# Kernel optimization log

Measured on AMD Instinct MI355X. Metric: run time of the kernel, lower is better.

## Reference

```python
import jax, jax.numpy as jnp
import numpy as np

TEMP = 0.07
LOSS_WEIGHT = 0.01
QSIZE = 1024


def _l2norm(x, axis):
    # torch: x / clamp_min(norm(x, dim=axis, keepdim=True), 1e-5)
    return x / jnp.maximum(jnp.linalg.norm(x, axis=axis, keepdims=True), 1e-5)


def setup_inputs() -> dict:
    key = jax.random.key(0)
    k1, k2, k3, k4 = jax.random.split(key, 4)
    B, E, H, W, C = 2, 256, 32, 32, 80
    feature = jax.random.normal(k1, (B, E, H, W), jnp.float32)
    u = jax.random.uniform(k2, (B, C, H, W), jnp.float32)
    center_map = jnp.where(u > 0.99, u, 0.0)
    score_map = jax.random.normal(k3, (B, C, H, W), jnp.float32)
    # buffer init: normalize(randn(Q,E,C), dim=1) / 10
    q = jax.random.normal(k4, (QSIZE, E, C), jnp.float32)
    queue = q / jnp.clip(jnp.linalg.norm(q, axis=1, keepdims=True), 1e-12) / 10.0
    return {"feature": feature, "center_map": center_map, "score_map": score_map, "queue": queue}


def reference(feature, center_map, score_map, queue):
    B, E, H, W = feature.shape
    C = score_map.shape[1]
    Class = center_map.shape[1]  # == C (required by the original assert)
    HW = H * W
    Q = queue.shape[0]  # steady state: queue_is_full -> Q = queue_size

    # score_map already at (H, W); nearest interpolate is identity
    sm = jax.lax.stop_gradient(score_map.reshape(B, C, HW).transpose(0, 2, 1))  # (B,HW,C)
    sm = jax.nn.softmax(sm / 0.001, axis=-1)
    cm = jax.lax.stop_gradient(center_map.reshape(B, Class, HW).transpose(0, 2, 1))  # (B,HW,Class)

    feat = feature.reshape(B, E, HW)
    # per-class prototypes from softmaxed score map, L2-normalized over E
    cate_protos = _l2norm(jnp.einsum('beh,bhc->bec', feat, sm), axis=1)  # (B,E,C)
    # update_queue: swap oldest batch (ptr=0) with detached current prototypes
    queue = queue.at[:B].set(jax.lax.stop_gradient(cate_protos))  # (Q,E,C)

    pos_proto = _l2norm(jnp.einsum('beh,bhk->bek', feat, cm), axis=1)  # (B,E,Class)
    feat_n = _l2norm(feat, axis=1)  # (B,E,HW)

    # feat_neg_score: (B, HW, Q, C); column (q,c) of the original (E, Q*C) view
    neg = jnp.einsum('beh,qec->bhqc', feat_n, queue) / TEMP
    pos = jnp.einsum('beh,bek->bhk', feat_n, pos_proto) / TEMP  # (B,HW,Class)

    # logsumexp over queue slots per class column
    s = jax.scipy.special.logsumexp(neg, axis=2)  # (B,HW,C)
    # for class cls, negatives exclude all columns with c == cls (pos_idx mask)
    eye = jnp.eye(C, dtype=bool)  # (cls, c)
    s_excl = jnp.where(eye[None, None], -jnp.inf, s[:, :, None, :])  # (B,HW,cls,c)
    lse_neg = jax.scipy.special.logsumexp(s_excl, axis=-1)  # (B,HW,C)
    # concat logits = [l_pos, masked negs]; total logsumexp
    lse_total = jnp.logaddexp(pos, lse_neg)  # (B,HW,C)

    # labels = cls (faithful to original code): in the concat ordering, index cls is
    # l_pos for cls==0, else masked-neg column (q=0, c=cls-1)
    tgt = jnp.concatenate([pos[:, :, :1], neg[:, :, 0, :C - 1]], axis=-1)  # (B,HW,C)
    ce = lse_total - tgt  # per-pixel, per-class CE

    mask = (cm > 0).astype(ce.dtype)  # (B,HW,Class)
    cnt = mask.sum(axis=(0, 1))  # (Class,)
    per_cls = jnp.where(cnt > 0, (ce * mask).sum(axis=(0, 1)) / jnp.maximum(cnt, 1.0), 0.0)
    return LOSS_WEIGHT * per_cls.sum()
```

## Files before the change

kernel.cpp:

```cpp
#include <hip/hip_runtime.h>
#include <hip/hip_bf16.h>


#define B_ 2
#define E_ 256
#define HW_ 1024
#define C_ 80
#define Q_ 1024

typedef __attribute__((ext_vector_type(4))) float f32x4;
typedef __attribute__((ext_vector_type(8))) short bf16x8;
typedef unsigned int u32;
typedef __attribute__((ext_vector_type(4))) u32 u32x4;

#define L2E 1.4426950408889634f
#define SCALE_A (L2E / 0.07f)
#define INV_TEMP (1.0f / 0.07f)

__device__ __forceinline__ ushort f2bf(float f) {
  union { __hip_bfloat16 b; ushort u; } cv;
  cv.b = __float2bfloat16(f);
  return cv.u;
}

__device__ __forceinline__ void gload_lds16(const short* g, short* l) {
  __builtin_amdgcn_global_load_lds(
      (const __attribute__((address_space(1))) void*)g,
      (__attribute__((address_space(3))) void*)l, 16, 0, 0);
}

__device__ __forceinline__ float wred_sum(float v) {
#pragma unroll
  for (int m = 1; m < 64; m <<= 1) v += __shfl_xor(v, m, 64);
  return v;
}

__global__ void k_sm(const float* __restrict__ score, float* __restrict__ SM,
                     float* __restrict__ CSUM, float* __restrict__ CCNT) {
  __shared__ float ld[80][33];
  __shared__ float red[8][32];
  __shared__ float mstore[32], istore[32];
  int t = threadIdx.x;
  if (blockIdx.x == 0 && t < C_) { CSUM[t] = 0.f; CCNT[t] = 0.f; }
  int p0 = blockIdx.x * 32;
  int b = p0 >> 10, h0 = p0 & 1023;
#pragma unroll
  for (int j = 0; j < 3; j++) {
    int idx = j*256 + t;
    if (idx < 640) {
      int row = idx >> 3, c4 = idx & 7;
      float4 v = *(const float4*)(score + ((size_t)(b*C_ + row))*HW_ + h0 + c4*4);
      ld[row][c4*4+0] = v.x; ld[row][c4*4+1] = v.y;
      ld[row][c4*4+2] = v.z; ld[row][c4*4+3] = v.w;
    }
  }
  __syncthreads();
  int px = t & 31, wg = t >> 5;
  float m = -__builtin_inff();
  for (int c = wg*10; c < wg*10 + 10; c++) m = fmaxf(m, ld[c][px]);
  red[wg][px] = m;
  __syncthreads();
  if (t < 32) {
    float mm = red[0][t];
#pragma unroll
    for (int g = 1; g < 8; g++) mm = fmaxf(mm, red[g][t]);
    mstore[t] = mm;
  }
  __syncthreads();
  float mf = mstore[px];
  float s = 0.f;
  for (int c = wg*10; c < wg*10 + 10; c++)
    s += __builtin_amdgcn_exp2f((ld[c][px] - mf) * (1000.0f * L2E));
  red[wg][px] = s;
  __syncthreads();
  if (t < 32) {
    float ss = 0.f;
#pragma unroll
    for (int g = 0; g < 8; g++) ss += red[g][t];
    istore[t] = 1.0f / ss;
  }
  __syncthreads();
#pragma unroll
  for (int j = 0; j < 3; j++) {
    int idx = j*256 + t;
    if (idx < 640) {
      int wpx = idx / 20, c4 = idx % 20;
      float mf2 = mstore[wpx], iv = istore[wpx];
      float4 o;
      o.x = __builtin_amdgcn_exp2f((ld[c4*4+0][wpx] - mf2) * (1000.0f * L2E)) * iv;
      o.y = __builtin_amdgcn_exp2f((ld[c4*4+1][wpx] - mf2) * (1000.0f * L2E)) * iv;
      o.z = __builtin_amdgcn_exp2f((ld[c4*4+2][wpx] - mf2) * (1000.0f * L2E)) * iv;
      o.w = __builtin_amdgcn_exp2f((ld[c4*4+3][wpx] - mf2) * (1000.0f * L2E)) * iv;
      *(float4*)(SM + (size_t)(p0 + wpx)*C_ + c4*4) = o;
    }
  }
}

__global__ void k_featn(const float* __restrict__ feat, float* __restrict__ FEATN,
                        float* __restrict__ NORM, __hip_bfloat16* __restrict__ ABF) {
  __shared__ float ld[256][33];
  __shared__ float red[8][32];
  __shared__ float istore[32];
  int t = threadIdx.x;
  int p0 = blockIdx.x * 32;
  int b = p0 >> 10, h0 = p0 & 1023;
#pragma unroll
  for (int j = 0; j < 8; j++) {
    int idx = j*256 + t;
    int row = idx >> 3, c4 = idx & 7;
    float4 v = *(const float4*)(feat + ((size_t)(b*E_ + row))*HW_ + h0 + c4*4);
    ld[row][c4*4+0] = v.x; ld[row][c4*4+1] = v.y;
    ld[row][c4*4+2] = v.z; ld[row][c4*4+3] = v.w;
  }
  __syncthreads();
  int px = t & 31, wg = t >> 5;
  float s = 0.f;
  for (int e = wg*32; e < wg*32 + 32; e++) { float v = ld[e][px]; s += v*v; }
  red[wg][px] = s;
  __syncthreads();
  if (t < 32) {
    float ss = 0.f;
#pragma unroll
    for (int g = 0; g < 8; g++) ss += red[g][t];
    float nrm = sqrtf(ss);
    NORM[p0 + t] = nrm;
    istore[t] = 1.0f / fmaxf(nrm, 1e-5f);
  }
  __syncthreads();
#pragma unroll
  for (int j = 0; j < 8; j++) {
    int idx = j*256 + t;
    int wpx = idx >> 6, e4 = idx & 63;
    float iv = istore[wpx];
    float f0 = ld[e4*4+0][wpx] * iv;
    float f1 = ld[e4*4+1][wpx] * iv;
    float f2 = ld[e4*4+2][wpx] * iv;
    float f3 = ld[e4*4+3][wpx] * iv;
    float4 o; o.x = f0; o.y = f1; o.z = f2; o.w = f3;
    *(float4*)(FEATN + (size_t)(p0 + wpx)*E_ + e4*4) = o;
    ushort4 pk;
    pk.x = f2bf(f0 * SCALE_A); pk.y = f2bf(f1 * SCALE_A);
    pk.z = f2bf(f2 * SCALE_A); pk.w = f2bf(f3 * SCALE_A);
    *(ushort4*)((ushort*)ABF + (size_t)(p0 + wpx)*E_ + e4*4) = pk;
  }
}

__global__ void k_protos(const float* __restrict__ SM, const float* __restrict__ cmap,
                         const float* __restrict__ FEATN, const float* __restrict__ NORM,
                         float* __restrict__ PART) {
  int hch = blockIdx.x, b = blockIdx.y;
  int map = blockIdx.z >> 1, ch = blockIdx.z & 1;
  int e = threadIdx.x;
  __shared__ float wl[64][40];
  for (int idx = threadIdx.x; idx < 64*40; idx += 256) {
    int ii = idx / 40, cl = idx % 40;
    int c = ch*40 + cl;
    int p = b*HW_ + hch*64 + ii;
    int h = p & 1023;
    float wv = (map == 0) ? SM[(size_t)p*C_ + c] : cmap[((size_t)(b*C_ + c))*HW_ + h];
    wl[ii][cl] = wv * NORM[p];
  }
  __syncthreads();
  float acc[40];
#pragma unroll
  for (int j = 0; j < 40; j++) acc[j] = 0.f;
  for (int ii = 0; ii < 64; ii++) {
    int p = b*HW_ + hch*64 + ii;
    float f = FEATN[(size_t)p*E_ + e];
#pragma unroll
    for (int j = 0; j < 40; j++) acc[j] += f * wl[ii][j];
  }
  float* out = PART + ((size_t)(hch*4 + map*2 + b)*E_ + e)*C_ + ch*40;
#pragma unroll
  for (int j = 0; j < 40; j++) out[j] = acc[j];
}

__global__ void k_protred(const float* __restrict__ PART, float* __restrict__ PROT) {
  int g = blockIdx.x*256 + threadIdx.x;
  float s = 0.f;
#pragma unroll 8
  for (int chk = 0; chk < 32; chk++) s += PART[(size_t)chk*81920 + g];
  PROT[g] = s;
}

__global__ void k_norm(float* PROT) {
  int w = threadIdx.x >> 6, l = threadIdx.x & 63;
  int gid = blockIdx.x*4 + w;
  int mb = gid / C_, c = gid % C_;
  float v[4]; float ss = 0.f;
#pragma unroll
  for (int i = 0; i < 4; i++) {
    v[i] = PROT[((size_t)(mb*E_ + l + 64*i))*C_ + c];
    ss += v[i]*v[i];
  }
  ss = wred_sum(ss);
  float inv = 1.0f / fmaxf(sqrtf(ss), 1e-5f);
#pragma unroll
  for (int i = 0; i < 4; i++)
    PROT[((size_t)(mb*E_ + l + 64*i))*C_ + c] = v[i]*inv;
}

__global__ void k_transpose(const float* __restrict__ queue,
                            __hip_bfloat16* __restrict__ QB) {
  __shared__ float ld[64*81];
  int q = blockIdx.x, t = threadIdx.x;
  if (q < B_) {
    bf16x8 z = (bf16x8){0,0,0,0,0,0,0,0};
    for (int i = t; i < C_*E_/8; i += 256) {
      int c = i >> 5, chunk = i & 31;
      *(bf16x8*)(QB + ((size_t)c*Q_ + q)*E_ + chunk*8) = z;
    }
    return;
  }
  const float* src = queue + (size_t)q*E_*C_;
  for (int ec = 0; ec < 4; ec++) {
    for (int i = t; i < 1280; i += 256) {
      float4 v = *(const float4*)(src + (size_t)ec*5120 + (size_t)i*4);
      int row = i / 20, col = (i % 20) * 4;
      ld[row*81 + col + 0] = v.x; ld[row*81 + col + 1] = v.y;
      ld[row*81 + col + 2] = v.z; ld[row*81 + col + 3] = v.w;
    }
    __syncthreads();
#pragma unroll
    for (int pass = 0; pass < 5; pass++) {
      int c = pass*16 + (t >> 4);
      int el = t & 15;
      ushort4 pack;
      pack.x = f2bf(ld[(el*4 + 0)*81 + c]);
      pack.y = f2bf(ld[(el*4 + 1)*81 + c]);
      pack.z = f2bf(ld[(el*4 + 2)*81 + c]);
      pack.w = f2bf(ld[(el*4 + 3)*81 + c]);
      *(ushort4*)(QB + ((size_t)c*Q_ + q)*E_ + ec*64 + el*4) = pack;
    }
    __syncthreads();
  }
}

__launch_bounds__(256, 2)
__global__ void k_gemm(const short* __restrict__ A, const short* __restrict__ QB,
                       float* __restrict__ SE) {
  __shared__ short Bs[2][128*64];
  __shared__ float xred[2][4][4][4];
  const int tid = threadIdx.x;
  const int l = tid & 63, w = tid >> 6;
  const int wr = w >> 1, wc = w & 1;
  const int fq = l >> 4, lr = l & 15;
  int bid = blockIdx.x;
  int wid = (bid & 7) * 160 + (bid >> 3);
  const int mt = wid & 15, cls = wid >> 4;
  const short* Bq = QB + (size_t)cls * (Q_ * E_);

  bf16x8 a[4][8];
  {
    const short* Ab = A + ((size_t)(mt*128 + wr*64 + lr)) * 256 + fq*8;
#pragma unroll
    for (int mi = 0; mi < 4; mi++)
#pragma unroll
      for (int kk = 0; kk < 8; kk++)
        a[mi][kk] = *(const bf16x8*)(Ab + mi*16*256 + kk*32);
  }

  int bgoff[4];
#pragma unroll
  for (int i = 0; i < 4; i++) {
    int s = i*256 + tid;
    int row = s >> 3, cp = s & 7;
    bgoff[i] = row*256 + ((cp ^ row) & 7)*8;
  }
  int boff[4][2];
#pragma unroll
  for (int ni = 0; ni < 4; ni++) {
    int rowb = wc*64 + ni*16 + lr;
#pragma unroll
    for (int ksub = 0; ksub < 2; ksub++)
      boff[ni][ksub] = rowb*64 + (((ksub*4 + fq) ^ rowb) & 7)*8;
  }

  f32x4 acc[4][4];
  float rs[4][4];
#pragma unroll
  for (int mi = 0; mi < 4; mi++)
#pragma unroll
    for (int ni = 0; ni < 4; ni++) acc[mi][ni] = (f32x4){0.f,0.f,0.f,0.f};
#pragma unroll
  for (int mi = 0; mi < 4; mi++)
#pragma unroll
    for (int j = 0; j < 4; j++) rs[mi][j] = 0.f;

#define BSRC(U, I) (Bq + (size_t)((U) >> 2) * 32768 + ((U) & 3) * 64 + bgoff[I])
#define STAGEB(U, BUF) { _Pragma("unroll") for (int i = 0; i < 4; i++) \
    gload_lds16(BSRC(U, i), &Bs[BUF][0] + (i*256 + w*64)*8); }

  STAGEB(0, 0);
  __syncthreads();

  for (int u4 = 0; u4 < 8; u4++) {
#pragma unroll
    for (int ks = 0; ks < 4; ks++) {
      const int u = u4*4 + ks;
      const int cur = ks & 1;
      if (u < 31) STAGEB(u+1, cur ^ 1);
#pragma unroll
      for (int ksub = 0; ksub < 2; ksub++) {
        const int kk = ks*2 + ksub;
        bf16x8 bfr[4];
#pragma unroll
        for (int ni = 0; ni < 4; ni++) bfr[ni] = *(const bf16x8*)(&Bs[cur][0] + boff[ni][ksub]);
#pragma unroll
        for (int mi = 0; mi < 4; mi++)
#pragma unroll
          for (int ni = 0; ni < 4; ni++)
            acc[mi][ni] = __builtin_amdgcn_mfma_f32_16x16x32_bf16(a[mi][kk], bfr[ni], acc[mi][ni], 0, 0, 0);
      }
      if (ks == 3) {
#pragma unroll
        for (int mi = 0; mi < 4; mi++)
#pragma unroll
          for (int j = 0; j < 4; j++) {
            float s = 0.f;
#pragma unroll
            for (int ni = 0; ni < 4; ni++) s += __builtin_amdgcn_exp2f(acc[mi][ni][j]);
            rs[mi][j] += s;
#pragma unroll
            for (int ni = 0; ni < 4; ni++) acc[mi][ni][j] = 0.f;
          }
      }
      __syncthreads();
    }
  }
#undef BSRC
#undef STAGEB

#pragma unroll
  for (int mi = 0; mi < 4; mi++)
#pragma unroll
    for (int j = 0; j < 4; j++) {
      float x = rs[mi][j];
      x += __shfl_xor(x, 1, 64);
      x += __shfl_xor(x, 2, 64);
      x += __shfl_xor(x, 4, 64);
      x += __shfl_xor(x, 8, 64);
      rs[mi][j] = x;
    }
  if (wc == 1 && lr == 0) {
#pragma unroll
    for (int mi = 0; mi < 4; mi++)
#pragma unroll
      for (int j = 0; j < 4; j++) xred[wr][mi][fq][j] = rs[mi][j];
  }
  __syncthreads();
  if (wc == 0 && lr == 0) {
#pragma unroll
    for (int mi = 0; mi < 4; mi++)
#pragma unroll
      for (int j = 0; j < 4; j++) {
        int p = mt*128 + wr*64 + mi*16 + fq*4 + j;
        SE[(size_t)p * C_ + cls] = rs[mi][j] + xred[wr][mi][fq][j];
      }
  }
}

__global__ void k_lossf(const float* __restrict__ FEATN, const float* __restrict__ PROT,
                        const float* __restrict__ SE, const float* __restrict__ cmap,
                        float* __restrict__ CSUM, float* __restrict__ CCNT) {
  __shared__ float lf[4][E_];
  int w = threadIdx.x >> 6, l = threadIdx.x & 63;
  int p = blockIdx.x * 4 + w;
  int b = p >> 10, h = p & 1023;
  float4 v = *(const float4*)(FEATN + (size_t)p*E_ + l*4);
  lf[w][l*4+0] = v.x; lf[w][l*4+1] = v.y; lf[w][l*4+2] = v.z; lf[w][l*4+3] = v.w;
  __syncthreads();
  const float* Ppos  = PROT + (size_t)(2 + b)*E_*C_;
  const float* Pneg0 = PROT;
  const float* Pneg1 = PROT + (size_t)E_*C_;
  float ap[2] = {0.f, 0.f}, an0[2] = {0.f, 0.f}, an1[2] = {0.f, 0.f};
#pragma unroll
  for (int part = 0; part < 2; part++) {
    int cc = part*64 + l;
    if (cc < C_) {
      float a = 0.f, n0 = 0.f, n1 = 0.f;
#pragma unroll 8
      for (int e = 0; e < E_; e++) {
        float f = lf[w][e];
        a  += f * Ppos [(size_t)e*C_ + cc];
        n0 += f * Pneg0[(size_t)e*C_ + cc];
        n1 += f * Pneg1[(size_t)e*C_ + cc];
      }
      ap[part] = a * INV_TEMP; an0[part] = n0 * INV_TEMP; an1[part] = n1 * INV_TEMP;
    }
  }
  float pos0    = __shfl(ap[0], 0, 64);
  float n0m1_p0 = __shfl(an0[0], (l + 63) & 63, 64);
  float n0m1_p1 = __shfl(an0[1], (l + 63) & 63, 64);
  float n0_63   = __shfl(an0[0], 63, 64);
  float full0 = SE[(size_t)p*C_ + l] - 2.0f + expf(an0[0]) + expf(an1[0]);
  float full1 = (l < C_ - 64)
              ? SE[(size_t)p*C_ + 64 + l] - 2.0f + expf(an0[1]) + expf(an1[1]) : 0.f;
  float T = wred_sum(full0 + full1);
#pragma unroll
  for (int part = 0; part < 2; part++) {
    int cc = part*64 + l;
    if (cc < C_) {
      float cmv = cmap[((size_t)(b*C_ + cc))*HW_ + h];
      if (cmv > 0.f) {
        float se = part ? full1 : full0;
        float pc = ap[part];
        float tgt = (part == 0) ? ((cc == 0) ? pos0 : n0m1_p0)
                                : ((l == 0) ? n0_63 : n0m1_p1);
        float ce = logf(expf(pc) + (T - se)) - tgt;
        atomicAdd(&CSUM[cc], ce);
        atomicAdd(&CCNT[cc], 1.0f);
      }
    }
  }
}

__global__ void k_final(const float* __restrict__ CSUM, const float* __restrict__ CCNT,
                        float* __restrict__ out) {
  int l = threadIdx.x;
  float s = 0.f;
  for (int c = l; c < C_; c += 64) {
    float cnt = CCNT[c];
    if (cnt > 0.f) s += CSUM[c] / fmaxf(cnt, 1.0f);
  }
  s = wred_sum(s);
  if (l == 0) out[0] = 0.01f * s;
}

static constexpr size_t OFF_SM    = 0;
static constexpr size_t OFF_PROT  = OFF_SM    + 655360;
static constexpr size_t OFF_FEATN = OFF_PROT  + 327680;
static constexpr size_t OFF_NORM  = OFF_FEATN + 2097152;
static constexpr size_t OFF_ABF   = OFF_NORM  + 8192;
static constexpr size_t OFF_SE    = OFF_ABF   + 1048576;
static constexpr size_t OFF_CSUM  = OFF_SE    + 655360;
static constexpr size_t OFF_CCNT  = OFF_CSUM  + 512;
static constexpr size_t OFF_PART  = OFF_CCNT  + 512;
static constexpr size_t OFF_QB    = OFF_PART  + 10485760;
static constexpr size_t WS_NEED   = OFF_QB    + 41943040;

extern "C" void kernel_launch(void* const* d_in, const int* in_sizes, int n_in,
                              void* d_out, int out_size, void* d_ws, size_t ws_size,
                              hipStream_t stream) {
  (void)in_sizes; (void)n_in; (void)out_size;
  if (ws_size < WS_NEED) return;

  const float* feature = (const float*)d_in[0];
  const float* cmap    = (const float*)d_in[1];
  const float* score   = (const float*)d_in[2];
  const float* queue   = (const float*)d_in[3];
  float* out = (float*)d_out;

  char* ws = (char*)d_ws;
  float* SM    = (float*)(ws + OFF_SM);
  float* PROT  = (float*)(ws + OFF_PROT);
  float* FEATN = (float*)(ws + OFF_FEATN);
  float* NORM  = (float*)(ws + OFF_NORM);
  __hip_bfloat16* ABF = (__hip_bfloat16*)(ws + OFF_ABF);
  float* SE    = (float*)(ws + OFF_SE);
  float* CSUM  = (float*)(ws + OFF_CSUM);
  float* CCNT  = (float*)(ws + OFF_CCNT);
  float* PART  = (float*)(ws + OFF_PART);
  __hip_bfloat16* QB = (__hip_bfloat16*)(ws + OFF_QB);

  k_sm<<<64, 256, 0, stream>>>(score, SM, CSUM, CCNT);
  k_featn<<<64, 256, 0, stream>>>(feature, FEATN, NORM, ABF);
  k_protos<<<dim3(32, 2, 4), 256, 0, stream>>>(SM, cmap, FEATN, NORM, PART);
  k_protred<<<320, 256, 0, stream>>>(PART, PROT);
  k_norm<<<80, 256, 0, stream>>>(PROT);
  k_transpose<<<1024, 256, 0, stream>>>(queue, QB);
  k_gemm<<<1280, 256, 0, stream>>>((const short*)ABF, (const short*)QB, SE);
  k_lossf<<<512, 256, 0, stream>>>(FEATN, PROT, SE, cmap, CSUM, CCNT);
  k_final<<<1, 64, 0, stream>>>(CSUM, CCNT, out);
}
```

Before: 183.9 us.

## Merge prep kernels into one launch and triple-buffer GEMM B tiles

Three preprocessing kernels (softmax, feature normalization, queue transpose to bf16) are merged into a single launch that dispatches on block index. This removes two kernel launches and lets the independent work run concurrently. The GEMM goes from double to triple buffering of the B tile, prefetching two stages ahead. It replaces __syncthreads with explicit vmcnt waits plus raw barriers and raises wave priority around the MFMA section. Triple buffering increases LDS use to about 48KB per block, which may reduce occupancy, and the hand-placed waitcnt logic is fragile.

```diff
diff --git a/kernel.cpp b/kernel.cpp
--- a/kernel.cpp
+++ b/kernel.cpp
@@ -35,113 +35,157 @@
   return v;
 }
 
-__global__ void k_sm(const float* __restrict__ score, float* __restrict__ SM,
-                     float* __restrict__ CSUM, float* __restrict__ CCNT) {
-  __shared__ float ld[80][33];
-  __shared__ float red[8][32];
-  __shared__ float mstore[32], istore[32];
-  int t = threadIdx.x;
-  if (blockIdx.x == 0 && t < C_) { CSUM[t] = 0.f; CCNT[t] = 0.f; }
-  int p0 = blockIdx.x * 32;
-  int b = p0 >> 10, h0 = p0 & 1023;
-#pragma unroll
-  for (int j = 0; j < 3; j++) {
-    int idx = j*256 + t;
-    if (idx < 640) {
+__global__ void k_prep(const float* __restrict__ score, const float* __restrict__ feature,
+                       const float* __restrict__ queue, float* __restrict__ SM,
+                       float* __restrict__ FEATN, float* __restrict__ NORM,
+                       __hip_bfloat16* __restrict__ ABF, __hip_bfloat16* __restrict__ QB,
+                       float* __restrict__ CSUM, float* __restrict__ CCNT) {
+  __shared__ float smem[8768];
+  const int gb = blockIdx.x;
+  const int t = threadIdx.x;
+
+  if (gb < 1024) {
+    float* ld = smem;
+    int q = gb;
+    if (q < B_) {
+      bf16x8 z = (bf16x8){0,0,0,0,0,0,0,0};
+      for (int i = t; i < C_*E_/8; i += 256) {
+        int c = i >> 5, chunk = i & 31;
+        *(bf16x8*)(QB + ((size_t)c*Q_ + q)*E_ + chunk*8) = z;
+      }
+      return;
+    }
+    const float* src = queue + (size_t)q*E_*C_;
+    for (int ec = 0; ec < 4; ec++) {
+      for (int i = t; i < 1280; i += 256) {
+        float4 v = *(const float4*)(src + (size_t)ec*5120 + (size_t)i*4);
+        int row = i / 20, col = (i % 20) * 4;
+        ld[row*81 + col + 0] = v.x; ld[row*81 + col + 1] = v.y;
+        ld[row*81 + col + 2] = v.z; ld[row*81 + col + 3] = v.w;
+      }
+      __syncthreads();
+#pragma unroll
+      for (int pass = 0; pass < 5; pass++) {
+        int c = pass*16 + (t >> 4);
+        int el = t & 15;
+        ushort4 pack;
+        pack.x = f2bf(ld[(el*4 + 0)*81 + c]);
+        pack.y = f2bf(ld[(el*4 + 1)*81 + c]);
+        pack.z = f2bf(ld[(el*4 + 2)*81 + c]);
+        pack.w = f2bf(ld[(el*4 + 3)*81 + c]);
+        *(ushort4*)(QB + ((size_t)c*Q_ + q)*E_ + ec*64 + el*4) = pack;
+      }
+      __syncthreads();
+    }
+    return;
+  }
+
+  if (gb < 1088) {
+    float* ld = smem;
+    float* red = smem + 8448;
+    float* istore = smem + 8704;
+    int p0 = (gb - 1024) * 32;
+    int b = p0 >> 10, h0 = p0 & 1023;
+#pragma unroll
+    for (int j = 0; j < 8; j++) {
+      int idx = j*256 + t;
       int row = idx >> 3, c4 = idx & 7;
-      float4 v = *(const float4*)(score + ((size_t)(b*C_ + row))*HW_ + h0 + c4*4);
-      ld[row][c4*4+0] = v.x; ld[row][c4*4+1] = v.y;
-      ld[row][c4*4+2] = v.z; ld[row][c4*4+3] = v.w;
-    }
-  }
-  __syncthreads();
-  int px = t & 31, wg = t >> 5;
-  float m = -__builtin_inff();
-  for (int c = wg*10; c < wg*10 + 10; c++) m = fmaxf(m, ld[c][px]);
-  red[wg][px] = m;
-  __syncthreads();
-  if (t < 32) {
-    float mm = red[0][t];
-#pragma unroll
-    for (int g = 1; g < 8; g++) mm = fmaxf(mm, red[g][t]);
-    mstore[t] = mm;
-  }
-  __syncthreads();
-  float mf = mstore[px];
-  float s = 0.f;
-  for (int c = wg*10; c < wg*10 + 10; c++)
-    s += __builtin_amdgcn_exp2f((ld[c][px] - mf) * (1000.0f * L2E));
-  red[wg][px] = s;
-  __syncthreads();
-  if (t < 32) {
-    float ss = 0.f;
-#pragma unroll
-    for (int g = 0; g < 8; g++) ss += red[g][t];
-    istore[t] = 1.0f / ss;
-  }
-  __syncthreads();
-#pragma unroll
-  for (int j = 0; j < 3; j++) {
-    int idx = j*256 + t;
-    if (idx < 640) {
-      int wpx = idx / 20, c4 = idx % 20;
-      float mf2 = mstore[wpx], iv = istore[wpx];
-      float4 o;
-      o.x = __builtin_amdgcn_exp2f((ld[c4*4+0][wpx] - mf2) * (1000.0f * L2E)) * iv;
-      o.y = __builtin_amdgcn_exp2f((ld[c4*4+1][wpx] - mf2) * (1000.0f * L2E)) * iv;
-      o.z = __builtin_amdgcn_exp2f((ld[c4*4+2][wpx] - mf2) * (1000.0f * L2E)) * iv;
-      o.w = __builtin_amdgcn_exp2f((ld[c4*4+3][wpx] - mf2) * (1000.0f * L2E)) * iv;
-      *(float4*)(SM + (size_t)(p0 + wpx)*C_ + c4*4) = o;
-    }
-  }
-}
-
-__global__ void k_featn(const float* __restrict__ feat, float* __restrict__ FEATN,
-                        float* __restrict__ NORM, __hip_bfloat16* __restrict__ ABF) {
-  __shared__ float ld[256][33];
-  __shared__ float red[8][32];
-  __shared__ float istore[32];
-  int t = threadIdx.x;
-  int p0 = blockIdx.x * 32;
-  int b = p0 >> 10, h0 = p0 & 1023;
-#pragma unroll
-  for (int j = 0; j < 8; j++) {
-    int idx = j*256 + t;
-    int row = idx >> 3, c4 = idx & 7;
-    float4 v = *(const float4*)(feat + ((size_t)(b*E_ + row))*HW_ + h0 + c4*4);
-    ld[row][c4*4+0] = v.x; ld[row][c4*4+1] = v.y;
-    ld[row][c4*4+2] = v.z; ld[row][c4*4+3] = v.w;
-  }
-  __syncthreads();
-  int px = t & 31, wg = t >> 5;
-  float s = 0.f;
-  for (int e = wg*32; e < wg*32 + 32; e++) { float v = ld[e][px]; s += v*v; }
-  red[wg][px] = s;
-  __syncthreads();
-  if (t < 32) {
-    float ss = 0.f;
-#pragma unroll
-    for (int g = 0; g < 8; g++) ss += red[g][t];
-    float nrm = sqrtf(ss);
-    NORM[p0 + t] = nrm;
-    istore[t] = 1.0f / fmaxf(nrm, 1e-5f);
-  }
-  __syncthreads();
-#pragma unroll
-  for (int j = 0; j < 8; j++) {
-    int idx = j*256 + t;
-    int wpx = idx >> 6, e4 = idx & 63;
-    float iv = istore[wpx];
-    float f0 = ld[e4*4+0][wpx] * iv;
-    float f1 = ld[e4*4+1][wpx] * iv;
-    float f2 = ld[e4*4+2][wpx] * iv;
-    float f3 = ld[e4*4+3][wpx] * iv;
-    float4 o; o.x = f0; o.y = f1; o.z = f2; o.w = f3;
-    *(float4*)(FEATN + (size_t)(p0 + wpx)*E_ + e4*4) = o;
-    ushort4 pk;
-    pk.x = f2bf(f0 * SCALE_A); pk.y = f2bf(f1 * SCALE_A);
-    pk.z = f2bf(f2 * SCALE_A); pk.w = f2bf(f3 * SCALE_A);
-    *(ushort4*)((ushort*)ABF + (size_t)(p0 + wpx)*E_ + e4*4) = pk;
+      float4 v = *(const float4*)(feature + ((size_t)(b*E_ + row))*HW_ + h0 + c4*4);
+      ld[row*33 + c4*4+0] = v.x; ld[row*33 + c4*4+1] = v.y;
+      ld[row*33 + c4*4+2] = v.z; ld[row*33 + c4*4+3] = v.w;
+    }
+    __syncthreads();
+    int px = t & 31, wg = t >> 5;
+    float s = 0.f;
+    for (int e = wg*32; e < wg*32 + 32; e++) { float v = ld[e*33 + px]; s += v*v; }
+    red[wg*32 + px] = s;
+    __syncthreads();
+    if (t < 32) {
+      float ss = 0.f;
+#pragma unroll
+      for (int g = 0; g < 8; g++) ss += red[g*32 + t];
+      float nrm = sqrtf(ss);
+      NORM[p0 + t] = nrm;
+      istore[t] = 1.0f / fmaxf(nrm, 1e-5f);
+    }
+    __syncthreads();
+#pragma unroll
+    for (int j = 0; j < 8; j++) {
+      int idx = j*256 + t;
+      int wpx = idx >> 6, e4 = idx & 63;
+      float iv = istore[wpx];
+      float f0 = ld[(e4*4+0)*33 + wpx] * iv;
+      float f1 = ld[(e4*4+1)*33 + wpx] * iv;
+      float f2 = ld[(e4*4+2)*33 + wpx] * iv;
+      float f3 = ld[(e4*4+3)*33 + wpx] * iv;
+      float4 o; o.x = f0; o.y = f1; o.z = f2; o.w = f3;
+      *(float4*)(FEATN + (size_t)(p0 + wpx)*E_ + e4*4) = o;
+      ushort4 pk;
+      pk.x = f2bf(f0 * SCALE_A); pk.y = f2bf(f1 * SCALE_A);
+      pk.z = f2bf(f2 * SCALE_A); pk.w = f2bf(f3 * SCALE_A);
+      *(ushort4*)((ushort*)ABF + (size_t)(p0 + wpx)*E_ + e4*4) = pk;
+    }
+    return;
+  }
+
+  {
+    float* ld = smem;
+    float* red = smem + 2640;
+    float* mstore = smem + 2896;
+    float* istore = smem + 2928;
+    if (gb == 1088 && t < C_) { CSUM[t] = 0.f; CCNT[t] = 0.f; }
+    int p0 = (gb - 1088) * 32;
+    int b = p0 >> 10, h0 = p0 & 1023;
+#pragma unroll
+    for (int j = 0; j < 3; j++) {
+      int idx = j*256 + t;
+      if (idx < 640) {
+        int row = idx >> 3, c4 = idx & 7;
+        float4 v = *(const float4*)(score + ((size_t)(b*C_ + row))*HW_ + h0 + c4*4);
+        ld[row*33 + c4*4+0] = v.x; ld[row*33 + c4*4+1] = v.y;
+        ld[row*33 + c4*4+2] = v.z; ld[row*33 + c4*4+3] = v.w;
+      }
+    }
+    __syncthreads();
+    int px = t & 31, wg = t >> 5;
+    float m = -__builtin_inff();
+    for (int c = wg*10; c < wg*10 + 10; c++) m = fmaxf(m, ld[c*33 + px]);
+    red[wg*32 + px] = m;
+    __syncthreads();
+    if (t < 32) {
+      float mm = red[t];
+#pragma unroll
+      for (int g = 1; g < 8; g++) mm = fmaxf(mm, red[g*32 + t]);
+      mstore[t] = mm;
+    }
+    __syncthreads();
+    float mf = mstore[px];
+    float s = 0.f;
+    for (int c = wg*10; c < wg*10 + 10; c++)
+      s += __builtin_amdgcn_exp2f((ld[c*33 + px] - mf) * (1000.0f * L2E));
+    red[wg*32 + px] = s;
+    __syncthreads();
+    if (t < 32) {
+      float ss = 0.f;
+#pragma unroll
+      for (int g = 0; g < 8; g++) ss += red[g*32 + t];
+      istore[t] = 1.0f / ss;
+    }
+    __syncthreads();
+#pragma unroll
+    for (int j = 0; j < 3; j++) {
+      int idx = j*256 + t;
+      if (idx < 640) {
+        int wpx = idx / 20, c4 = idx % 20;
+        float mf2 = mstore[wpx], iv = istore[wpx];
+        float4 o;
+        o.x = __builtin_amdgcn_exp2f((ld[(c4*4+0)*33 + wpx] - mf2) * (1000.0f * L2E)) * iv;
+        o.y = __builtin_amdgcn_exp2f((ld[(c4*4+1)*33 + wpx] - mf2) * (1000.0f * L2E)) * iv;
+        o.z = __builtin_amdgcn_exp2f((ld[(c4*4+2)*33 + wpx] - mf2) * (1000.0f * L2E)) * iv;
+        o.w = __builtin_amdgcn_exp2f((ld[(c4*4+3)*33 + wpx] - mf2) * (1000.0f * L2E)) * iv;
+        *(float4*)(SM + (size_t)(p0 + wpx)*C_ + c4*4) = o;
+      }
+    }
   }
 }
 
@@ -200,46 +244,10 @@
     PROT[((size_t)(mb*E_ + l + 64*i))*C_ + c] = v[i]*inv;
 }
 
-__global__ void k_transpose(const float* __restrict__ queue,
-                            __hip_bfloat16* __restrict__ QB) {
-  __shared__ float ld[64*81];
-  int q = blockIdx.x, t = threadIdx.x;
-  if (q < B_) {
-    bf16x8 z = (bf16x8){0,0,0,0,0,0,0,0};
-    for (int i = t; i < C_*E_/8; i += 256) {
-      int c = i >> 5, chunk = i & 31;
-      *(bf16x8*)(QB + ((size_t)c*Q_ + q)*E_ + chunk*8) = z;
-    }
-    return;
-  }
-  const float* src = queue + (size_t)q*E_*C_;
-  for (int ec = 0; ec < 4; ec++) {
-    for (int i = t; i < 1280; i += 256) {
-      float4 v = *(const float4*)(src + (size_t)ec*5120 + (size_t)i*4);
-      int row = i / 20, col = (i % 20) * 4;
-      ld[row*81 + col + 0] = v.x; ld[row*81 + col + 1] = v.y;
-      ld[row*81 + col + 2] = v.z; ld[row*81 + col + 3] = v.w;
-    }
-    __syncthreads();
-#pragma unroll
-    for (int pass = 0; pass < 5; pass++) {
-      int c = pass*16 + (t >> 4);
-      int el = t & 15;
-      ushort4 pack;
-      pack.x = f2bf(ld[(el*4 + 0)*81 + c]);
-      pack.y = f2bf(ld[(el*4 + 1)*81 + c]);
-      pack.z = f2bf(ld[(el*4 + 2)*81 + c]);
-      pack.w = f2bf(ld[(el*4 + 3)*81 + c]);
-      *(ushort4*)(QB + ((size_t)c*Q_ + q)*E_ + ec*64 + el*4) = pack;
-    }
-    __syncthreads();
-  }
-}
-
 __launch_bounds__(256, 2)
 __global__ void k_gemm(const short* __restrict__ A, const short* __restrict__ QB,
                        float* __restrict__ SE) {
-  __shared__ short Bs[2][128*64];
+  __shared__ short Bs[3][128*64];
   __shared__ float xred[2][4][4][4];
   const int tid = threadIdx.x;
   const int l = tid & 63, w = tid >> 6;
@@ -289,29 +297,36 @@
 
 #define BSRC(U, I) (Bq + (size_t)((U) >> 2) * 32768 + ((U) & 3) * 64 + bgoff[I])
 #define STAGEB(U, BUF) { _Pragma("unroll") for (int i = 0; i < 4; i++) \
-    gload_lds16(BSRC(U, i), &Bs[BUF][0] + (i*256 + w*64)*8); }
+    gload_lds16(BSRC(U, i), &Bs[0][0] + (BUF)*(128*64) + (i*256 + w*64)*8); }
+#define VMCNT4 asm volatile("s_waitcnt vmcnt(4)" ::: "memory")
+#define VMCNT0 asm volatile("s_waitcnt vmcnt(0)" ::: "memory")
 
   STAGEB(0, 0);
-  __syncthreads();
+  STAGEB(1, 1);
+  VMCNT4;
+  __builtin_amdgcn_s_barrier();
 
   for (int u4 = 0; u4 < 8; u4++) {
 #pragma unroll
     for (int ks = 0; ks < 4; ks++) {
       const int u = u4*4 + ks;
-      const int cur = ks & 1;
-      if (u < 31) STAGEB(u+1, cur ^ 1);
+      const int cur = u % 3;
+      if (ks < 2 || u4 < 7) STAGEB(u+2, (u+2) % 3);
+      const short* Bcur = &Bs[0][0] + cur*(128*64);
+      __builtin_amdgcn_s_setprio(1);
 #pragma unroll
       for (int ksub = 0; ksub < 2; ksub++) {
         const int kk = ks*2 + ksub;
         bf16x8 bfr[4];
 #pragma unroll
-        for (int ni = 0; ni < 4; ni++) bfr[ni] = *(const bf16x8*)(&Bs[cur][0] + boff[ni][ksub]);
+        for (int ni = 0; ni < 4; ni++) bfr[ni] = *(const bf16x8*)(Bcur + boff[ni][ksub]);
 #pragma unroll
         for (int mi = 0; mi < 4; mi++)
 #pragma unroll
           for (int ni = 0; ni < 4; ni++)
             acc[mi][ni] = __builtin_amdgcn_mfma_f32_16x16x32_bf16(a[mi][kk], bfr[ni], acc[mi][ni], 0, 0, 0);
       }
+      __builtin_amdgcn_s_setprio(0);
       if (ks == 3) {
 #pragma unroll
         for (int mi = 0; mi < 4; mi++)
@@ -325,11 +340,20 @@
             for (int ni = 0; ni < 4; ni++) acc[mi][ni][j] = 0.f;
           }
       }
-      __syncthreads();
+      if (ks < 2) {
+        VMCNT4; __builtin_amdgcn_s_barrier();
+      } else if (ks == 2) {
+        if (u4 < 7) { VMCNT4; } else { VMCNT0; }
+        __builtin_amdgcn_s_barrier();
+      } else {
+        if (u4 < 7) { VMCNT4; __builtin_amdgcn_s_barrier(); }
+      }
     }
   }
 #undef BSRC
 #undef STAGEB
+#undef VMCNT4
+#undef VMCNT0
 
 #pragma unroll
   for (int mi = 0; mi < 4; mi++)
@@ -463,12 +487,10 @@
   float* PART  = (float*)(ws + OFF_PART);
   __hip_bfloat16* QB = (__hip_bfloat16*)(ws + OFF_QB);
 
-  k_sm<<<64, 256, 0, stream>>>(score, SM, CSUM, CCNT);
-  k_featn<<<64, 256, 0, stream>>>(feature, FEATN, NORM, ABF);
+  k_prep<<<1152, 256, 0, stream>>>(score, feature, queue, SM, FEATN, NORM, ABF, QB, CSUM, CCNT);
   k_protos<<<dim3(32, 2, 4), 256, 0, stream>>>(SM, cmap, FEATN, NORM, PART);
   k_protred<<<320, 256, 0, stream>>>(PART, PROT);
   k_norm<<<80, 256, 0, stream>>>(PROT);
-  k_transpose<<<1024, 256, 0, stream>>>(queue, QB);
   k_gemm<<<1280, 256, 0, stream>>>((const short*)ABF, (const short*)QB, SE);
   k_lossf<<<512, 256, 0, stream>>>(FEATN, PROT, SE, cmap, CSUM, CCNT);
   k_final<<<1, 64, 0, stream>>>(CSUM, CCNT, out);
```

Measured after the change: 192.1 us. 1.04x slower.
